# Kernel tuning notes

Hardware: AMD Instinct MI355X
Metric: run time of the kernel (lower is better)

## Reference

```python
import jax, jax.numpy as jnp
import numpy as np

B, S, DIM = 16, 8192, 128
H, KV, D = 4, 2, 64  # heads, kv_heads, dim_head


def setup_inputs() -> dict:
    key = jax.random.key(0)
    ks = jax.random.split(key, 8)
    scale = 0.05
    return {
        "x": jax.random.normal(ks[0], (B, S, DIM), dtype=jnp.float32),
        "Wq": jax.random.normal(ks[1], (H, D, DIM), dtype=jnp.float32) * scale,
        "bq": jax.random.normal(ks[2], (H, D), dtype=jnp.float32) * scale,
        "Wk": jax.random.normal(ks[3], (KV, D, DIM), dtype=jnp.float32) * scale,
        "bk": jax.random.normal(ks[4], (KV, D), dtype=jnp.float32) * scale,
        "Wv": jax.random.normal(ks[5], (KV, D, DIM), dtype=jnp.float32) * scale,
        "bv": jax.random.normal(ks[6], (KV, D), dtype=jnp.float32) * scale,
        "Wo": jax.random.normal(ks[7], (DIM, DIM), dtype=jnp.float32) * scale,
    }


def reference(x, Wq, bq, Wk, bk, Wv, bv, Wo):
    b, s, _ = x.shape
    # MultiHeadLinear: per-head Linear stacked on last axis -> [B,S,D,H]
    q_st = jnp.einsum("bsc,hdc->bsdh", x, Wq) + bq.T  # [B,S,D,H]
    k_st = jnp.einsum("bsc,hdc->bsdh", x, Wk) + bk.T  # [B,S,D,KV]
    v_st = jnp.einsum("bsc,hdc->bsdh", x, Wv) + bv.T  # [B,S,D,KV]
    # .view(B,-1,heads,dim_head): raw reshape of (D,H) block into (H,D)
    q = q_st.reshape(b, s, H, D)
    k = k_st.reshape(b, s, KV, D)
    v = v_st.reshape(b, s, KV, D)
    # k scaled by q mean over heads (no softmax anywhere)
    k = k * jnp.mean(q, axis=2, keepdims=True)  # [B,S,KV,D]
    attn = jnp.einsum("bshd,bskd->bshk", q, k) / jnp.sqrt(jnp.asarray(D, q.dtype))
    out = jnp.einsum("bshk,bskd->bshd", attn, v)  # [B,S,H,D]
    # reshape(B,-1,dim): [B,S,H*D=256] -> [B,2S,128]
    out = out.reshape(b, -1, DIM)
    return out @ Wo.T
```

## Files before the change

kernel.cpp:

```cpp
#include <hip/hip_runtime.h>
#include <stdint.h>


using short8 = __attribute__((ext_vector_type(8))) short;
using f32x4  = __attribute__((ext_vector_type(4))) float;
using f32x2  = __attribute__((ext_vector_type(2))) float;

constexpr int XSTR = 136;
constexpr int PSTR = 10;
constexpr int T_TILES = 8;

__device__ __forceinline__ unsigned short f2bf(float f) {
    unsigned int u = __float_as_uint(f);
    u += 0x7FFFu + ((u >> 16) & 1u);
    return (unsigned short)(u >> 16);
}

__device__ __forceinline__ void barrier_nodrain() {
    asm volatile("s_waitcnt lgkmcnt(0)\n\ts_barrier" ::: "memory");
}

__global__ void prep_weights(const float* __restrict__ Wq, const float* __restrict__ bq,
                             const float* __restrict__ Wk, const float* __restrict__ bk,
                             const float* __restrict__ Wv, const float* __restrict__ bv,
                             const float* __restrict__ Wo,
                             unsigned short* __restrict__ Wp, float* __restrict__ bias)
{
    const int ch = blockIdx.x;
    const int c  = threadIdx.x;
    float w, b;
    if (ch < 256) {
        const int hh = ch & 3, dd = ch >> 2;
        w = Wq[(hh * 64 + dd) * 128 + c];
        b = bq[hh * 64 + dd];
    } else if (ch < 384) {
        const int i = ch - 256;
        const int kvh = i & 1, dd = i >> 1;
        w = Wk[(kvh * 64 + dd) * 128 + c];
        b = bk[kvh * 64 + dd];
    } else {
        const int i  = ch - 384;
        const int jg = i >> 6, kp = (i >> 4) & 3, jm = i & 15;
        const int j  = (jg >> 1) * 32 + jm * 2 + (jg & 1);
        const int kv = kp >> 1, p = kp & 1;
        float acc = 0.f, bacc = 0.f;
        #pragma unroll 8
        for (int d = 0; d < 64; ++d) {
            const int idx = kv * 64 + d;
            const int kvh = idx & 1, dd = idx >> 1;
            const float wo = Wo[j * 128 + p * 64 + d];
            acc  += wo * Wv[(kvh * 64 + dd) * 128 + c];
            bacc += wo * bv[kvh * 64 + dd];
        }
        w = acc; b = bacc;
    }
    Wp[ch * 128 + c] = f2bf(w);
    if (c == 0) bias[ch] = b;
}

__device__ __forceinline__ void stage8_load(const float* __restrict__ x, int tb, int row0,
                                            int l, f32x4* xv)
{
    const int row = row0 + (l >> 3);
    const f32x4* src = (const f32x4*)(x + (size_t)(tb + row) * 128) + (l & 7);
    #pragma unroll
    for (int j = 0; j < 4; ++j) xv[j] = __builtin_nontemporal_load(src + 8 * j);
}
__device__ __forceinline__ void stage8_write(unsigned short* __restrict__ xb, int row0,
                                             int l, const f32x4* xv)
{
    const int row = row0 + (l >> 3);
    #pragma unroll
    for (int j = 0; j < 4; ++j) {
        ushort4 s;
        s.x = f2bf(xv[j][0]); s.y = f2bf(xv[j][1]); s.z = f2bf(xv[j][2]); s.w = f2bf(xv[j][3]);
        *(ushort4*)&xb[row * XSTR + (l & 7) * 4 + 32 * j] = s;
    }
}

__global__ __launch_bounds__(512, 2)
void fused_attn_kernel(const float* __restrict__ x,
                       const unsigned short* __restrict__ Wp,
                       const float* __restrict__ bias,
                       float* __restrict__ out)
{
    __shared__ __align__(16) unsigned short xlds[3][64 * XSTR];
    __shared__ __align__(16) float partial[2][4][64][PSTR];
    __shared__ __align__(16) float coeffw[4][64][8];

    const int tid = threadIdx.x;
    const int l   = tid & 63;
    const int wv  = tid >> 6;
    const int lr  = l & 15, lg = l >> 4;
    const int tok0 = blockIdx.x * (T_TILES * 64);

    if (wv < 4) {
        const int dc = wv;
        const int row0 = dc * 8;
        int chb[6];
        #pragma unroll
        for (int n = 0; n < 4; ++n) chb[n] = n * 64 + dc * 16;
        chb[4] = 256 + dc * 16;
        chb[5] = 320 + dc * 16;

        short8 areg[24];
        #pragma unroll
        for (int n = 0; n < 6; ++n)
            #pragma unroll
            for (int ks = 0; ks < 4; ++ks)
                areg[n * 4 + ks] = *(const short8*)(Wp + (size_t)(chb[n] + lr) * 128 + ks * 32 + lg * 8);
        f32x4 biasv[6];
        #pragma unroll
        for (int n = 0; n < 6; ++n)
            biasv[n] = *(const f32x4*)(bias + chb[n] + lg * 4);

        auto phase1 = [&](const unsigned short* __restrict__ xb, int pb) {
            #pragma unroll
            for (int p = 0; p < 4; ++p) {
                f32x4 acc[6];
                #pragma unroll
                for (int n = 0; n < 6; ++n) acc[n] = (f32x4){0.f, 0.f, 0.f, 0.f};
                __builtin_amdgcn_s_setprio(1);
                #pragma unroll
                for (int ks = 0; ks < 4; ++ks) {
                    short8 bfr = *(const short8*)&xb[(p * 16 + lr) * XSTR + ks * 32 + lg * 8];
                    #pragma unroll
                    for (int n = 0; n < 6; ++n)
                        acc[n] = __builtin_amdgcn_mfma_f32_16x16x32_bf16(
                            areg[n * 4 + ks], bfr, acc[n], 0, 0, 0);
                }
                __builtin_amdgcn_s_setprio(0);
                float pa[8];
                #pragma unroll
                for (int c = 0; c < 8; ++c) pa[c] = 0.f;
                #pragma unroll
                for (int r = 0; r < 4; ++r) {
                    const float q0 = acc[0][r] + biasv[0][r];
                    const float q1 = acc[1][r] + biasv[1][r];
                    const float q2 = acc[2][r] + biasv[2][r];
                    const float q3 = acc[3][r] + biasv[3][r];
                    const float k0v = acc[4][r] + biasv[4][r];
                    const float k1v = acc[5][r] + biasv[5][r];
                    const float qm  = 0.25f * (q0 + q1 + q2 + q3);
                    const float kt0 = k0v * qm, kt1 = k1v * qm;
                    pa[0] += q0 * kt0; pa[1] += q1 * kt0;
                    pa[2] += q0 * kt1; pa[3] += q1 * kt1;
                    pa[4] += q2 * kt0; pa[5] += q3 * kt0;
                    pa[6] += q2 * kt1; pa[7] += q3 * kt1;
                }
                #pragma unroll
                for (int c = 0; c < 8; ++c) pa[c] += __shfl_xor(pa[c], 16);
                #pragma unroll
                for (int c = 0; c < 8; ++c) pa[c] += __shfl_xor(pa[c], 32);
                if (lg == 0) {
                    float* dst = &partial[pb][dc][p * 16 + lr][0];
                    *(float2*)(dst)     = make_float2(pa[0], pa[1]);
                    *(float2*)(dst + 2) = make_float2(pa[2], pa[3]);
                    *(float2*)(dst + 4) = make_float2(pa[4], pa[5]);
                    *(float2*)(dst + 6) = make_float2(pa[6], pa[7]);
                }
            }
        };

        f32x4 xv[4];
        stage8_load(x, tok0, row0, l, xv);
        stage8_write(xlds[0], row0, l, xv);
        stage8_load(x, tok0 + 64, row0, l, xv);
        barrier_nodrain();
        phase1(xlds[0], 0);

        for (int t = 0; t < T_TILES; ++t) {
            stage8_write(xlds[(t + 1) % 3], row0, l, xv);
            const int tl = (t + 2 < T_TILES) ? t + 2 : T_TILES - 1;
            stage8_load(x, tok0 + tl * 64, row0, l, xv);
            barrier_nodrain();
            if (t + 1 < T_TILES)
                phase1(xlds[(t + 1) % 3], (t + 1) & 1);
        }
    } else {
        const int jgp  = wv - 4;
        const int row0 = 32 + jgp * 8;

        short8 breg[32];
        #pragma unroll
        for (int j2 = 0; j2 < 2; ++j2)
            #pragma unroll
            for (int kp = 0; kp < 4; ++kp)
                #pragma unroll
                for (int ks = 0; ks < 4; ++ks)
                    breg[(j2 * 4 + kp) * 4 + ks] = *(const short8*)
                        (Wp + (size_t)(384 + (jgp * 2 + j2) * 64 + kp * 16 + lr) * 128 + ks * 32 + lg * 8);
        float bvv[2][4];
        #pragma unroll
        for (int j2 = 0; j2 < 2; ++j2)
            #pragma unroll
            for (int kp = 0; kp < 4; ++kp)
                bvv[j2][kp] = bias[384 + (jgp * 2 + j2) * 64 + kp * 16 + lr];

        f32x4 xv[4];
        stage8_load(x, tok0, row0, l, xv);
        stage8_write(xlds[0], row0, l, xv);
        stage8_load(x, tok0 + 64, row0, l, xv);
        barrier_nodrain();

        for (int t = 0; t < T_TILES; ++t) {
            stage8_write(xlds[(t + 1) % 3], row0, l, xv);
            const int tl = (t + 2 < T_TILES) ? t + 2 : T_TILES - 1;
            stage8_load(x, tok0 + tl * 64, row0, l, xv);
            barrier_nodrain();

            {
                const int pb = t & 1;
                float s[8];
                #pragma unroll
                for (int c = 0; c < 8; ++c) s[c] = 0.f;
                #pragma unroll
                for (int dcc = 0; dcc < 4; ++dcc) {
                    const float* pr = &partial[pb][dcc][l][0];
                    #pragma unroll
                    for (int c = 0; c < 4; ++c) {
                        float2 v = *(const float2*)(pr + 2 * c);
                        s[2 * c] += v.x; s[2 * c + 1] += v.y;
                    }
                }
                float* cw = &coeffw[jgp][l][0];
                *(float2*)(cw)     = make_float2(s[0] * 0.125f, s[1] * 0.125f);
                *(float2*)(cw + 2) = make_float2(s[2] * 0.125f, s[3] * 0.125f);
                *(float2*)(cw + 4) = make_float2(s[4] * 0.125f, s[5] * 0.125f);
                *(float2*)(cw + 6) = make_float2(s[6] * 0.125f, s[7] * 0.125f);
            }

            {
                const unsigned short* xb = xlds[t % 3];
                const int g0    = tok0 + t * 64;
                const int bb    = g0 >> 13;
                const int srow0 = bb * 16384 + 2 * (g0 & 8191);
                #pragma unroll
                for (int mf = 0; mf < 4; ++mf) {
                    f32x4 a2[2][4];
                    #pragma unroll
                    for (int j2 = 0; j2 < 2; ++j2)
                        #pragma unroll
                        for (int kp = 0; kp < 4; ++kp)
                            a2[j2][kp] = (f32x4){0.f, 0.f, 0.f, 0.f};
                    __builtin_amdgcn_s_setprio(1);
                    #pragma unroll
                    for (int ks = 0; ks < 4; ++ks) {
                        short8 af = *(const short8*)&xb[(mf * 16 + lr) * XSTR + ks * 32 + lg * 8];
                        #pragma unroll
                        for (int j2 = 0; j2 < 2; ++j2)
                            #pragma unroll
                            for (int kp = 0; kp < 4; ++kp)
                                a2[j2][kp] = __builtin_amdgcn_mfma_f32_16x16x32_bf16(
                                    af, breg[(j2 * 4 + kp) * 4 + ks], a2[j2][kp], 0, 0, 0);
                    }
                    __builtin_amdgcn_s_setprio(0);
                    #pragma unroll
                    for (int r = 0; r < 4; ++r) {
                        const int tokL = lg * 4 + r;
                        const int tok  = mf * 16 + tokL;
                        f32x4 cl = *(const f32x4*)&coeffw[jgp][tok][0];
                        f32x4 ch = *(const f32x4*)&coeffw[jgp][tok][4];
                        f32x2 s0, s1;
                        {
                            const float a0 = a2[0][0][r] + bvv[0][0];
                            const float a1 = a2[0][1][r] + bvv[0][1];
                            const float av = a2[0][2][r] + bvv[0][2];
                            const float a3 = a2[0][3][r] + bvv[0][3];
                            s0[0] = cl[0] * a0 + cl[1] * a1 + cl[2] * av + cl[3] * a3;
                            s1[0] = ch[0] * a0 + ch[1] * a1 + ch[2] * av + ch[3] * a3;
                        }
                        {
                            const float a0 = a2[1][0][r] + bvv[1][0];
                            const float a1 = a2[1][1][r] + bvv[1][1];
                            const float av = a2[1][2][r] + bvv[1][2];
                            const float a3 = a2[1][3][r] + bvv[1][3];
                            s0[1] = cl[0] * a0 + cl[1] * a1 + cl[2] * av + cl[3] * a3;
                            s1[1] = ch[0] * a0 + ch[1] * a1 + ch[2] * av + ch[3] * a3;
                        }
                        const int row = srow0 + 32 * mf + 2 * tokL;
                        float* dst = out + (size_t)row * 128 + jgp * 32 + lr * 2;
                        __builtin_nontemporal_store(s0, (f32x2*)(dst));
                        __builtin_nontemporal_store(s1, (f32x2*)(dst + 128));
                    }
                }
            }
        }
    }
}

extern "C" void kernel_launch(void* const* d_in, const int* in_sizes, int n_in,
                              void* d_out, int out_size, void* d_ws, size_t ws_size,
                              hipStream_t stream)
{
    (void)in_sizes; (void)n_in; (void)out_size; (void)ws_size;
    const float* x  = (const float*)d_in[0];
    const float* Wq = (const float*)d_in[1];
    const float* bq = (const float*)d_in[2];
    const float* Wk = (const float*)d_in[3];
    const float* bk = (const float*)d_in[4];
    const float* Wv = (const float*)d_in[5];
    const float* bv = (const float*)d_in[6];
    const float* Wo = (const float*)d_in[7];

    unsigned short* Wp   = (unsigned short*)d_ws;
    float*          bias = (float*)((char*)d_ws + 896 * 128 * 2);

    prep_weights<<<896, 128, 0, stream>>>(Wq, bq, Wk, bk, Wv, bv, Wo, Wp, bias);
    fused_attn_kernel<<<256, 512, 0, stream>>>(x, Wp, bias, (float*)d_out);
}
```

Before: 61.36 us.

## Deepen x prefetch to two register stages and drop nontemporal hints and setprio

Result: slower. 77.50 us (+26.3%).

```diff
diff --git a/kernel.cpp b/kernel.cpp
--- a/kernel.cpp
+++ b/kernel.cpp
@@ -4,7 +4,6 @@
 
 using short8 = __attribute__((ext_vector_type(8))) short;
 using f32x4  = __attribute__((ext_vector_type(4))) float;
-using f32x2  = __attribute__((ext_vector_type(2))) float;
 
 constexpr int XSTR = 136;
 constexpr int PSTR = 10;
@@ -59,21 +58,21 @@
 }
 
 __device__ __forceinline__ void stage8_load(const float* __restrict__ x, int tb, int row0,
-                                            int l, f32x4* xv)
+                                            int l, float4* xv)
 {
     const int row = row0 + (l >> 3);
-    const f32x4* src = (const f32x4*)(x + (size_t)(tb + row) * 128) + (l & 7);
+    const float* src = x + (size_t)(tb + row) * 128 + (l & 7) * 4;
     #pragma unroll
-    for (int j = 0; j < 4; ++j) xv[j] = __builtin_nontemporal_load(src + 8 * j);
+    for (int j = 0; j < 4; ++j) xv[j] = *(const float4*)(src + 32 * j);
 }
 __device__ __forceinline__ void stage8_write(unsigned short* __restrict__ xb, int row0,
-                                             int l, const f32x4* xv)
+                                             int l, const float4* xv)
 {
     const int row = row0 + (l >> 3);
     #pragma unroll
     for (int j = 0; j < 4; ++j) {
         ushort4 s;
-        s.x = f2bf(xv[j][0]); s.y = f2bf(xv[j][1]); s.z = f2bf(xv[j][2]); s.w = f2bf(xv[j][3]);
+        s.x = f2bf(xv[j].x); s.y = f2bf(xv[j].y); s.z = f2bf(xv[j].z); s.w = f2bf(xv[j].w);
         *(ushort4*)&xb[row * XSTR + (l & 7) * 4 + 32 * j] = s;
     }
 }
@@ -120,7 +119,6 @@
                 f32x4 acc[6];
                 #pragma unroll
                 for (int n = 0; n < 6; ++n) acc[n] = (f32x4){0.f, 0.f, 0.f, 0.f};
-                __builtin_amdgcn_s_setprio(1);
                 #pragma unroll
                 for (int ks = 0; ks < 4; ++ks) {
                     short8 bfr = *(const short8*)&xb[(p * 16 + lr) * XSTR + ks * 32 + lg * 8];
@@ -129,7 +127,6 @@
                         acc[n] = __builtin_amdgcn_mfma_f32_16x16x32_bf16(
                             areg[n * 4 + ks], bfr, acc[n], 0, 0, 0);
                 }
-                __builtin_amdgcn_s_setprio(0);
                 float pa[8];
                 #pragma unroll
                 for (int c = 0; c < 8; ++c) pa[c] = 0.f;
@@ -162,20 +159,29 @@
             }
         };
 
-        f32x4 xv[4];
-        stage8_load(x, tok0, row0, l, xv);
-        stage8_write(xlds[0], row0, l, xv);
-        stage8_load(x, tok0 + 64, row0, l, xv);
+        float4 xvA[4], xvB[4];
+        stage8_load(x, tok0,       row0, l, xvA);
+        stage8_load(x, tok0 + 64,  row0, l, xvB);
+        stage8_write(xlds[0], row0, l, xvA);
+        stage8_load(x, tok0 + 128, row0, l, xvA);
+        stage8_write(xlds[1], row0, l, xvB);
+        stage8_load(x, tok0 + 192, row0, l, xvB);
         barrier_nodrain();
         phase1(xlds[0], 0);
+        barrier_nodrain();
 
         for (int t = 0; t < T_TILES; ++t) {
-            stage8_write(xlds[(t + 1) % 3], row0, l, xv);
-            const int tl = (t + 2 < T_TILES) ? t + 2 : T_TILES - 1;
-            stage8_load(x, tok0 + tl * 64, row0, l, xv);
-            barrier_nodrain();
+            const int tl = (t + 4 < T_TILES) ? t + 4 : T_TILES - 1;
+            if ((t & 1) == 0) {
+                stage8_write(xlds[(t + 2) % 3], row0, l, xvA);
+                stage8_load(x, tok0 + tl * 64, row0, l, xvA);
+            } else {
+                stage8_write(xlds[(t + 2) % 3], row0, l, xvB);
+                stage8_load(x, tok0 + tl * 64, row0, l, xvB);
+            }
             if (t + 1 < T_TILES)
                 phase1(xlds[(t + 1) % 3], (t + 1) & 1);
+            barrier_nodrain();
         }
     } else {
         const int jgp  = wv - 4;
@@ -197,17 +203,25 @@
             for (int kp = 0; kp < 4; ++kp)
                 bvv[j2][kp] = bias[384 + (jgp * 2 + j2) * 64 + kp * 16 + lr];
 
-        f32x4 xv[4];
-        stage8_load(x, tok0, row0, l, xv);
-        stage8_write(xlds[0], row0, l, xv);
-        stage8_load(x, tok0 + 64, row0, l, xv);
+        float4 xvA[4], xvB[4];
+        stage8_load(x, tok0,       row0, l, xvA);
+        stage8_load(x, tok0 + 64,  row0, l, xvB);
+        stage8_write(xlds[0], row0, l, xvA);
+        stage8_load(x, tok0 + 128, row0, l, xvA);
+        stage8_write(xlds[1], row0, l, xvB);
+        stage8_load(x, tok0 + 192, row0, l, xvB);
         barrier_nodrain();
+        barrier_nodrain();
 
         for (int t = 0; t < T_TILES; ++t) {
-            stage8_write(xlds[(t + 1) % 3], row0, l, xv);
-            const int tl = (t + 2 < T_TILES) ? t + 2 : T_TILES - 1;
-            stage8_load(x, tok0 + tl * 64, row0, l, xv);
-            barrier_nodrain();
+            const int tl = (t + 4 < T_TILES) ? t + 4 : T_TILES - 1;
+            if ((t & 1) == 0) {
+                stage8_write(xlds[(t + 2) % 3], row0, l, xvA);
+                stage8_load(x, tok0 + tl * 64, row0, l, xvA);
+            } else {
+                stage8_write(xlds[(t + 2) % 3], row0, l, xvB);
+                stage8_load(x, tok0 + tl * 64, row0, l, xvB);
+            }
 
             {
                 const int pb = t & 1;
@@ -243,7 +257,6 @@
                         #pragma unroll
                         for (int kp = 0; kp < 4; ++kp)
                             a2[j2][kp] = (f32x4){0.f, 0.f, 0.f, 0.f};
-                    __builtin_amdgcn_s_setprio(1);
                     #pragma unroll
                     for (int ks = 0; ks < 4; ++ks) {
                         short8 af = *(const short8*)&xb[(mf * 16 + lr) * XSTR + ks * 32 + lg * 8];
@@ -254,37 +267,37 @@
                                 a2[j2][kp] = __builtin_amdgcn_mfma_f32_16x16x32_bf16(
                                     af, breg[(j2 * 4 + kp) * 4 + ks], a2[j2][kp], 0, 0, 0);
                     }
-                    __builtin_amdgcn_s_setprio(0);
                     #pragma unroll
                     for (int r = 0; r < 4; ++r) {
                         const int tokL = lg * 4 + r;
                         const int tok  = mf * 16 + tokL;
                         f32x4 cl = *(const f32x4*)&coeffw[jgp][tok][0];
                         f32x4 ch = *(const f32x4*)&coeffw[jgp][tok][4];
-                        f32x2 s0, s1;
+                        float2 s0, s1;
                         {
                             const float a0 = a2[0][0][r] + bvv[0][0];
                             const float a1 = a2[0][1][r] + bvv[0][1];
                             const float av = a2[0][2][r] + bvv[0][2];
                             const float a3 = a2[0][3][r] + bvv[0][3];
-                            s0[0] = cl[0] * a0 + cl[1] * a1 + cl[2] * av + cl[3] * a3;
-                            s1[0] = ch[0] * a0 + ch[1] * a1 + ch[2] * av + ch[3] * a3;
+                            s0.x = cl[0] * a0 + cl[1] * a1 + cl[2] * av + cl[3] * a3;
+                            s1.x = ch[0] * a0 + ch[1] * a1 + ch[2] * av + ch[3] * a3;
                         }
                         {
                             const float a0 = a2[1][0][r] + bvv[1][0];
                             const float a1 = a2[1][1][r] + bvv[1][1];
                             const float av = a2[1][2][r] + bvv[1][2];
                             const float a3 = a2[1][3][r] + bvv[1][3];
-                            s0[1] = cl[0] * a0 + cl[1] * a1 + cl[2] * av + cl[3] * a3;
-                            s1[1] = ch[0] * a0 + ch[1] * a1 + ch[2] * av + ch[3] * a3;
+                            s0.y = cl[0] * a0 + cl[1] * a1 + cl[2] * av + cl[3] * a3;
+                            s1.y = ch[0] * a0 + ch[1] * a1 + ch[2] * av + ch[3] * a3;
                         }
                         const int row = srow0 + 32 * mf + 2 * tokL;
                         float* dst = out + (size_t)row * 128 + jgp * 32 + lr * 2;
-                        __builtin_nontemporal_store(s0, (f32x2*)(dst));
-                        __builtin_nontemporal_store(s1, (f32x2*)(dst + 128));
+                        *(float2*)(dst)       = s0;
+                        *(float2*)(dst + 128) = s1;
                     }
                 }
             }
+            barrier_nodrain();
         }
     }
 }
```
